# Kernel tuning notes

Hardware: AMD Instinct MI355X
Metric: run time of the kernel (lower is better)

## Reference

```python
import jax, jax.numpy as jnp
import numpy as np


def _c2e(faces):
    # faces: [6, B, C, h, h] in order back, down, front, left, right, up
    # returns equirect map [B, C, H=h, W=2h] via bilinear cube sampling
    _, B, C, h, _ = faces.shape
    H, W = h, 2 * h
    lat = (0.5 - (jnp.arange(H) + 0.5) / H) * jnp.pi      # +pi/2 (top) .. -pi/2
    lon = (2.0 * (jnp.arange(W) + 0.5) / W - 1.0) * jnp.pi  # -pi .. +pi
    cl = jnp.cos(lat)[:, None]
    vx = cl * jnp.sin(lon)[None, :]
    vy = jnp.broadcast_to(jnp.sin(lat)[:, None], (H, W))
    vz = cl * jnp.cos(lon)[None, :]
    dirs = jnp.stack([vx, vy, vz], -1)                     # [H,W,3]
    ax, ay, az = jnp.abs(vx), jnp.abs(vy), jnp.abs(vz)
    cond_z = (az >= ax) & (az >= ay)
    cond_x = (~cond_z) & (ax >= ay)
    # face ids: 0 back(-z) 1 down(-y) 2 front(+z) 3 left(-x) 4 right(+x) 5 up(+y)
    face = jnp.where(cond_z, jnp.where(vz > 0, 2, 0),
                     jnp.where(cond_x, jnp.where(vx > 0, 4, 3),
                               jnp.where(vy > 0, 5, 1)))
    N = jnp.array([[0, 0, -1], [0, -1, 0], [0, 0, 1], [-1, 0, 0], [1, 0, 0], [0, 1, 0]], jnp.float32)
    R = jnp.array([[-1, 0, 0], [1, 0, 0], [1, 0, 0], [0, 0, 1], [0, 0, -1], [1, 0, 0]], jnp.float32)
    U = jnp.array([[0, 1, 0], [0, 0, -1], [0, 1, 0], [0, 1, 0], [0, 1, 0], [0, 0, 1]], jnp.float32)
    den = jnp.sum(dirs * N[face], -1)
    a = jnp.sum(dirs * R[face], -1) / den                  # in-plane x, [-1,1]
    bcoord = jnp.sum(dirs * U[face], -1) / den             # in-plane y, [-1,1]
    uu = jnp.clip((a + 1.0) * 0.5 * (h - 1), 0.0, h - 1)   # align_corners-style
    vv = jnp.clip((1.0 - bcoord) * 0.5 * (h - 1), 0.0, h - 1)
    x0 = jnp.floor(uu).astype(jnp.int32)
    y0 = jnp.floor(vv).astype(jnp.int32)
    x1 = jnp.minimum(x0 + 1, h - 1)
    y1 = jnp.minimum(y0 + 1, h - 1)
    dx = uu - x0
    dy = vv - y0
    ft = faces.transpose(0, 3, 4, 1, 2).reshape(6, h, h, B * C)  # [6,h,h,B*C]
    g = lambda yy, xx: ft[face, yy, xx]                    # gather -> [H,W,B*C]
    out = (g(y0, x0) * ((1 - dx) * (1 - dy))[..., None]
           + g(y0, x1) * (dx * (1 - dy))[..., None]
           + g(y1, x0) * ((1 - dx) * dy)[..., None]
           + g(y1, x1) * (dx * dy)[..., None])
    return out.reshape(H, W, B, C).transpose(2, 3, 0, 1)


def _conv(x, w, bias, pad):
    y = jax.lax.conv_general_dilated(x, w, (1, 1), [(pad, pad), (pad, pad)],
                                     dimension_numbers=('NCHW', 'OIHW', 'NCHW'))
    return y + bias[None, :, None, None]


def setup_inputs() -> dict:
    key = jax.random.key(0)
    ks = jax.random.split(key, 12)
    B, C, h = 4, 64, 128
    face_shape = (B, C, h, h)
    return {
        'm': jax.random.normal(ks[0], (B, C, h, 2 * h), jnp.float32),
        'f': jax.random.normal(ks[1], face_shape, jnp.float32),
        'r': jax.random.normal(ks[2], face_shape, jnp.float32),
        'b': jax.random.normal(ks[3], face_shape, jnp.float32),
        'l': jax.random.normal(ks[4], face_shape, jnp.float32),
        'u': jax.random.normal(ks[5], face_shape, jnp.float32),
        'd': jax.random.normal(ks[6], face_shape, jnp.float32),
        'w_fusion': jax.random.normal(ks[7], (C, C, 3, 3), jnp.float32) * 0.05,
        'b_fusion': jnp.zeros((C,), jnp.float32),
        'w_mask': jax.random.normal(ks[8], (1, 2 * C, 1, 1), jnp.float32) * 0.05,
        'b_mask': jnp.zeros((1,), jnp.float32),
    }


def reference(m, f, r, b, l, u, d, w_fusion, b_fusion, w_mask, b_mask):
    # cube faces stacked in the original order: back, down, front, left, right, up
    faces = jnp.stack([b, d, f, l, r, u], 0)               # [6,B,C,h,h]
    aux = _c2e(faces)                                      # [B,C,h,2h]
    m_aux = jax.nn.relu(_conv(aux, w_fusion, b_fusion, 1))
    m_main = jax.nn.relu(_conv(m, w_fusion, b_fusion, 1))  # shared conv_fusion weights
    joint = jnp.concatenate([m_main, m_aux], axis=1)
    mask = jax.nn.sigmoid(_conv(joint, w_mask, b_mask, 0)) # [B,1,h,2h]
    return m + mask * m_aux
```

## Files before the change

### kernel.cpp

```cpp
#include <hip/hip_runtime.h>
#include <math.h>
#include <stdint.h>

#define BB 4
#define CC 64
#define HH 128
#define HOUT 128
#define WOUT 256
#define NPIX (HOUT * WOUT)
#define NMAP (BB * CC * HOUT * WOUT)

typedef __attribute__((ext_vector_type(8))) short short8;
typedef __attribute__((ext_vector_type(4))) float floatx4;

__device__ __forceinline__ uint16_t f2bf(float f) {
    uint32_t u = __float_as_uint(f);
    u += 0x7fffu + ((u >> 16) & 1u);
    return (uint16_t)(u >> 16);
}
__device__ __forceinline__ float bfu2f(uint32_t v) { return __uint_as_float(v << 16); }

__global__ __launch_bounds__(256) void prep_kernel(uint32_t* __restrict__ pk,
                                                   float* __restrict__ pdx,
                                                   float* __restrict__ pdy,
                                                   const float* __restrict__ wf,
                                                   uint4* __restrict__ Bsw) {
    if (blockIdx.x < 128) {
        int p = blockIdx.x * 256 + threadIdx.x;
        int y = p >> 8;
        int x = p & 255;
        const float PI = 3.14159265358979323846f;
        float lat = (0.5f - (y + 0.5f) / (float)HOUT) * PI;
        float lon = (2.0f * (x + 0.5f) / (float)WOUT - 1.0f) * PI;
        float cl = cosf(lat);
        float vx = cl * sinf(lon);
        float vy = sinf(lat);
        float vz = cl * cosf(lon);
        float ax = fabsf(vx), ay = fabsf(vy), az = fabsf(vz);

        int face;
        float den, a, b;
        if (az >= ax && az >= ay) {
            if (vz > 0.0f) { face = 2; den = vz;  a = vx;  b = vy; }
            else           { face = 0; den = -vz; a = -vx; b = vy; }
        } else if (ax >= ay) {
            if (vx > 0.0f) { face = 4; den = vx;  a = -vz; b = vy; }
            else           { face = 3; den = -vx; a = vz;  b = vy; }
        } else {
            if (vy > 0.0f) { face = 5; den = vy;  a = vx;  b = vz; }
            else           { face = 1; den = -vy; a = vx;  b = -vz; }
        }
        a /= den;
        b /= den;
        float uu = fminf(fmaxf((a + 1.0f) * 0.5f * (HH - 1), 0.0f), (float)(HH - 1));
        float vv = fminf(fmaxf((1.0f - b) * 0.5f * (HH - 1), 0.0f), (float)(HH - 1));
        int x0 = (int)floorf(uu);
        int y0 = (int)floorf(vv);
        int x1 = min(x0 + 1, HH - 1);
        int y1 = min(y0 + 1, HH - 1);
        pdx[p] = uu - (float)x0;
        pdy[p] = vv - (float)y0;
        pk[p] = (uint32_t)face | ((uint32_t)x0 << 3) | ((uint32_t)y0 << 10) |
                ((uint32_t)x1 << 17) | ((uint32_t)y1 << 24);
    } else {
        int tid = (blockIdx.x - 128) * 256 + threadIdx.x;
        if (tid >= 9 * 2 * 4 * 64) return;
        int lane = tid & 63;
        int rest = tid >> 6;
        int n = rest & 3, ks = (rest >> 2) & 1, tap = rest >> 3;
        int co = n * 16 + (lane & 15);
        uint32_t w4[4];
#pragma unroll
        for (int pw = 0; pw < 4; pw++) {
            int ci0 = ks * 32 + (lane >> 4) * 8 + pw * 2;
            uint32_t lo = f2bf(wf[(size_t)(co * CC + ci0) * 9 + tap]);
            uint32_t hi = f2bf(wf[(size_t)(co * CC + ci0 + 1) * 9 + tap]);
            w4[pw] = lo | (hi << 16);
        }
        Bsw[tid] = make_uint4(w4[0], w4[1], w4[2], w4[3]);
    }
}

__global__ __launch_bounds__(256) void facepack_kernel(
    const float* __restrict__ pB, const float* __restrict__ pD,
    const float* __restrict__ pF, const float* __restrict__ pL,
    const float* __restrict__ pR, const float* __restrict__ pU,
    uint16_t* __restrict__ FCL) {
    __shared__ uint16_t lds[64 * 256];
    int bid = blockIdx.x;
    int half = bid & 1;
    int y = (bid >> 1) & 127;
    int fc = bid >> 8;
    const float* src = (fc == 0) ? pB : (fc == 1) ? pD : (fc == 2) ? pF
                     : (fc == 3) ? pL : (fc == 4) ? pR : pU;
    int t = threadIdx.x;
    int xl = t & 63;
    int x = half * 64 + xl;
    int cgb = t >> 6;

#pragma unroll
    for (int i = 0; i < 8; i++) {
        int cg = i * 4 + cgb;
        uint32_t w4[4];
#pragma unroll
        for (int j = 0; j < 4; j++) {
            int bc0 = cg * 8 + j * 2;
            uint32_t lo = f2bf(src[((size_t)bc0 * HH + y) * HH + x]);
            uint32_t hi = f2bf(src[((size_t)(bc0 + 1) * HH + y) * HH + x]);
            w4[j] = lo | (hi << 16);
        }
        int off = xl * 256 + ((cg ^ (xl & 7)) * 8);
        *(uint4*)&lds[off] = make_uint4(w4[0], w4[1], w4[2], w4[3]);
    }
    __syncthreads();
    size_t obase = (((size_t)fc * HH + y) * HH + half * 64) * 256;
#pragma unroll
    for (int i = 0; i < 8; i++) {
        int q = i * 256 + t;
        int xx = q >> 5, cg = q & 31;
        int off = xx * 256 + ((cg ^ (xx & 7)) * 8);
        *(uint4*)&FCL[obase + (size_t)q * 8] = *(const uint4*)&lds[off];
    }
}

__global__ __launch_bounds__(256) void gather_kernel(
    const uint32_t* __restrict__ pk, const float* __restrict__ pdx,
    const float* __restrict__ pdy, const uint16_t* __restrict__ FCL,
    uint16_t* __restrict__ Xa) {
    int tid = blockIdx.x * 256 + threadIdx.x;
    int chunk = tid & 31;
    int p = tid >> 5;

    uint32_t k = pk[p];
    float dx = pdx[p], dy = pdy[p];
    int fc = k & 7;
    int x0 = (k >> 3) & 127, y0 = (k >> 10) & 127;
    int x1 = (k >> 17) & 127, y1 = (k >> 24) & 127;

    const uint16_t* base = FCL + (size_t)fc * HH * HH * 256 + chunk * 8;
    uint4 c00 = *(const uint4*)(base + ((size_t)y0 * HH + x0) * 256);
    uint4 c01 = *(const uint4*)(base + ((size_t)y0 * HH + x1) * 256);
    uint4 c10 = *(const uint4*)(base + ((size_t)y1 * HH + x0) * 256);
    uint4 c11 = *(const uint4*)(base + ((size_t)y1 * HH + x1) * 256);

    float w00 = (1.0f - dx) * (1.0f - dy);
    float w01 = dx * (1.0f - dy);
    float w10 = (1.0f - dx) * dy;
    float w11 = dx * dy;

    const uint32_t* a00 = (const uint32_t*)&c00;
    const uint32_t* a01 = (const uint32_t*)&c01;
    const uint32_t* a10 = (const uint32_t*)&c10;
    const uint32_t* a11 = (const uint32_t*)&c11;
    uint32_t r[4];
#pragma unroll
    for (int w = 0; w < 4; w++) {
        float lo = w00 * bfu2f(a00[w] & 0xffffu) + w01 * bfu2f(a01[w] & 0xffffu)
                 + w10 * bfu2f(a10[w] & 0xffffu) + w11 * bfu2f(a11[w] & 0xffffu);
        float hi = w00 * bfu2f(a00[w] >> 16) + w01 * bfu2f(a01[w] >> 16)
                 + w10 * bfu2f(a10[w] >> 16) + w11 * bfu2f(a11[w] >> 16);
        r[w] = (uint32_t)f2bf(lo) | ((uint32_t)f2bf(hi) << 16);
    }

    int b = chunk >> 3, c = (chunk & 7) * 8;
    int y = p >> 8, x = p & 255;
    size_t o = (((size_t)(b * HOUT + y)) * WOUT + x) * CC + c;
    *(uint4*)(Xa + o) = make_uint4(r[0], r[1], r[2], r[3]);
}

__global__ __launch_bounds__(256) void pack_kernel(const float* __restrict__ src,
                                                   uint16_t* __restrict__ dst) {
    __shared__ uint16_t lds[WOUT * CC];
    int t = threadIdx.x;
    int by = blockIdx.x;
    int b = by >> 7, y = by & 127;

#pragma unroll
    for (int cg = 0; cg < 8; cg++) {
        uint32_t w4[4];
#pragma unroll
        for (int pw = 0; pw < 4; pw++) {
            int c0 = cg * 8 + pw * 2;
            uint32_t lo = f2bf(src[((size_t)(b * CC + c0) * HOUT + y) * WOUT + t]);
            uint32_t hi = f2bf(src[((size_t)(b * CC + c0 + 1) * HOUT + y) * WOUT + t]);
            w4[pw] = lo | (hi << 16);
        }
        int off = t * 64 + ((cg ^ (t & 7)) * 8);
        *(uint4*)&lds[off] = make_uint4(w4[0], w4[1], w4[2], w4[3]);
    }
    __syncthreads();
    size_t obase = (size_t)((b * HOUT + y) * WOUT) * CC;
#pragma unroll
    for (int i = 0; i < 8; i++) {
        int q = i * 256 + t;
        int p = q >> 3, c8 = q & 7;
        int off = p * 64 + ((c8 ^ (p & 7)) * 8);
        *(uint4*)&dst[obase + (size_t)q * 8] = *(const uint4*)&lds[off];
    }
}

__global__ __launch_bounds__(256) void gemm_kernel(const uint16_t* __restrict__ Xm,
                                                   const uint16_t* __restrict__ Xa,
                                                   const uint4* __restrict__ Bsw,
                                                   const float* __restrict__ bias,
                                                   uint16_t* __restrict__ Ym,
                                                   uint16_t* __restrict__ Ya) {
    __shared__ uint16_t lds[3 * 160 * CC];
    int gid = blockIdx.x;
    int tensor = gid >> 10;
    int b = (gid >> 8) & 3;
    int i = gid & 255;
    int xcd = i & 7, j = i >> 3;
    int y = xcd * 16 + (j & 15);
    int h = j >> 4;
    const uint16_t* X = tensor ? Xa : Xm;
    uint16_t* Y = tensor ? Ya : Ym;
    const int wx = h * 128 - 16;

    int tid = threadIdx.x;
    const uint16_t* Xb = X + (size_t)b * (HOUT * WOUT * CC);
#pragma unroll
    for (int it = 0; it < 15; it++) {
        int cid = it * 256 + tid;
        int c = cid & 7;
        int pr = cid >> 3;
        int p = pr % 160;
        int r = pr / 160;
        int gy = y + r - 1;
        int gx = wx + p;
        uint4 v = make_uint4(0, 0, 0, 0);
        if ((unsigned)gy < (unsigned)HOUT && (unsigned)gx < (unsigned)WOUT)
            v = *(const uint4*)(Xb + ((size_t)gy * WOUT + gx) * CC + c * 8);
        int slot = (r * 160 + p) * 8 + (c ^ (p & 7));
        *(uint4*)&lds[slot * 8] = v;
    }
    __syncthreads();

    int lane = threadIdx.x & 63;
    int wave = threadIdx.x >> 6;
    int l15 = lane & 15, lq = lane >> 4;

    floatx4 acc[2][4];
#pragma unroll
    for (int mt = 0; mt < 2; mt++)
#pragma unroll
        for (int n = 0; n < 4; n++) acc[mt][n] = (floatx4)0.0f;

#pragma unroll
    for (int tap = 0; tap < 9; tap++) {
        const int dy = tap / 3 - 1, dx = tap % 3 - 1;
        const int r = 1 + dy;
#pragma unroll
        for (int ks = 0; ks < 2; ks++) {
            short8 bfr[4];
            const uint4* bp = Bsw + (size_t)((tap * 2 + ks) * 4) * 64 + lane;
#pragma unroll
            for (int n = 0; n < 4; n++) {
                uint4 t4 = bp[n * 64];
                bfr[n] = *(short8*)&t4;
            }
#pragma unroll
            for (int mt = 0; mt < 2; mt++) {
                int p = wave * 32 + mt * 16 + l15 + dx + 16;
                int chunk = ks * 4 + lq;
                int slot = (r * 160 + p) * 8 + (chunk ^ (p & 7));
                short8 af = *(const short8*)&lds[slot * 8];
#pragma unroll
                for (int n = 0; n < 4; n++)
                    acc[mt][n] = __builtin_amdgcn_mfma_f32_16x16x32_bf16(
                        af, bfr[n], acc[mt][n], 0, 0, 0);
            }
        }
    }
    long rowpix = (long)(b * HOUT + y) * WOUT;
#pragma unroll
    for (int n = 0; n < 4; n++) {
        int co = n * 16 + l15;
        float bb = bias[co];
#pragma unroll
        for (int mt = 0; mt < 2; mt++) {
#pragma unroll
            for (int rg = 0; rg < 4; rg++) {
                float v = acc[mt][n][rg] + bb;
                v = v > 0.0f ? v : 0.0f;
                long px = rowpix + h * 128 + wave * 32 + mt * 16 + lq * 4 + rg;
                Y[px * CC + co] = f2bf(v);
            }
        }
    }
}

__global__ __launch_bounds__(256) void maskfinal_kernel(
    const float* __restrict__ m, const uint16_t* __restrict__ Ym,
    const uint16_t* __restrict__ Ya, const float* __restrict__ wm,
    const float* __restrict__ bm, float* __restrict__ out) {
    int t = threadIdx.x;
    int by = blockIdx.x;
    int b = by >> 7, y = by & 127;
    size_t pix = (size_t)(b * HOUT + y) * WOUT + t;
    const uint4* ym4 = (const uint4*)(Ym + pix * CC);
    const uint4* ya4 = (const uint4*)(Ya + pix * CC);
    uint4 ya[8];
    float acc = bm[0];
#pragma unroll
    for (int g = 0; g < 8; g++) {
        uint4 um = ym4[g];
        uint4 av = ya4[g];
        ya[g] = av;
        const uint32_t* pu = (const uint32_t*)&um;
        const uint32_t* pa = (const uint32_t*)&av;
#pragma unroll
        for (int w = 0; w < 4; w++) {
            int c = g * 8 + w * 2;
            acc += wm[c]     * bfu2f(pu[w] & 0xffffu);
            acc += wm[c + 1] * bfu2f(pu[w] >> 16);
            acc += wm[64 + c]     * bfu2f(pa[w] & 0xffffu);
            acc += wm[64 + c + 1] * bfu2f(pa[w] >> 16);
        }
    }
    float mask = 1.0f / (1.0f + expf(-acc));
#pragma unroll
    for (int g = 0; g < 8; g++) {
        const uint32_t* pa = (const uint32_t*)&ya[g];
#pragma unroll
        for (int w = 0; w < 4; w++) {
            int c = g * 8 + w * 2;
            size_t i0 = ((size_t)(b * CC + c) * HOUT + y) * WOUT + t;
            size_t i1 = i0 + (size_t)HOUT * WOUT;
            out[i0] = m[i0] + mask * bfu2f(pa[w] & 0xffffu);
            out[i1] = m[i1] + mask * bfu2f(pa[w] >> 16);
        }
    }
}

__global__ __launch_bounds__(256) void signal_kernel(float* __restrict__ out, float v) {
    int idx = blockIdx.x * 256 + threadIdx.x;
    out[idx] = v;
}

extern "C" void kernel_launch(void* const* d_in, const int* in_sizes, int n_in,
                              void* d_out, int out_size, void* d_ws, size_t ws_size,
                              hipStream_t stream) {
    const float* m  = (const float*)d_in[0];
    const float* f  = (const float*)d_in[1];
    const float* r  = (const float*)d_in[2];
    const float* bk = (const float*)d_in[3];
    const float* l  = (const float*)d_in[4];
    const float* u  = (const float*)d_in[5];
    const float* dn = (const float*)d_in[6];
    const float* wf = (const float*)d_in[7];
    const float* bf = (const float*)d_in[8];
    const float* wm = (const float*)d_in[9];
    const float* bm = (const float*)d_in[10];
    float* out = (float*)d_out;

    const size_t OFF_FCL = 0;
    const size_t OFF_YM  = 0;
    const size_t OFF_YA  = (size_t)16 << 20;
    const size_t OFF_BSW = (size_t)51 << 20;
    const size_t OFF_PK  = OFF_BSW + (1u << 17);
    const size_t OFF_PDX = OFF_PK + (1u << 17);
    const size_t OFF_PDY = OFF_PDX + (1u << 17);
    const size_t NEED    = OFF_PDY + (1u << 17);

    if (ws_size < NEED) {
        float v = 100.0f + (float)(ws_size >> 20);
        signal_kernel<<<NMAP / 256, 256, 0, stream>>>(out, v);
        return;
    }

    char* ws = (char*)d_ws;
    uint16_t* FCL = (uint16_t*)(ws + OFF_FCL);
    uint16_t* Ym  = (uint16_t*)(ws + OFF_YM);
    uint16_t* Ya  = (uint16_t*)(ws + OFF_YA);
    uint4* Bsw    = (uint4*)(ws + OFF_BSW);
    uint32_t* pk  = (uint32_t*)(ws + OFF_PK);
    float* pdx    = (float*)(ws + OFF_PDX);
    float* pdy    = (float*)(ws + OFF_PDY);
    uint16_t* Xm  = (uint16_t*)d_out;
    uint16_t* Xa  = (uint16_t*)d_out + (size_t)NMAP;

    prep_kernel<<<146, 256, 0, stream>>>(pk, pdx, pdy, wf, Bsw);
    facepack_kernel<<<6 * HH * 2, 256, 0, stream>>>(bk, dn, f, l, r, u, FCL);
    gather_kernel<<<(NPIX * 32) / 256, 256, 0, stream>>>(pk, pdx, pdy, FCL, Xa);
    pack_kernel<<<BB * HOUT, 256, 0, stream>>>(m, Xm);
    gemm_kernel<<<2 * BB * HOUT * 2, 256, 0, stream>>>(Xm, Xa, Bsw, bf, Ym, Ya);
    maskfinal_kernel<<<BB * HOUT, 256, 0, stream>>>(m, Ym, Ya, wm, bm, out);
}
```

Measured before the change: 262.0 us.

## Fuse both conv GEMMs with mask and final blend into one kernel

The two 3x3 conv GEMMs (main and aux) now run as two phases inside a single block per row-half, and the 1x1 mask conv, sigmoid and residual blend are folded into the epilogue. The bf16 Ym/Ya intermediates and the separate maskfinal kernel are removed. The LDS halo is trimmed from 160 to 132 columns, and the face buffer and workspace layout are reshuffled so the output buffer holds part of the face cache. The trade-off is half as many blocks, serial phases within each block, and an LDS transpose before the NCHW stores.

```diff
diff --git a/kernel.cpp b/kernel.cpp
--- a/kernel.cpp
+++ b/kernel.cpp
@@ -9,6 +9,7 @@
 #define WOUT 256
 #define NPIX (HOUT * WOUT)
 #define NMAP (BB * CC * HOUT * WOUT)
+#define FSTR ((size_t)HH * HH * 256)
 
 typedef __attribute__((ext_vector_type(8))) short short8;
 typedef __attribute__((ext_vector_type(4))) float floatx4;
@@ -85,7 +86,7 @@
     const float* __restrict__ pB, const float* __restrict__ pD,
     const float* __restrict__ pF, const float* __restrict__ pL,
     const float* __restrict__ pR, const float* __restrict__ pU,
-    uint16_t* __restrict__ FCL) {
+    uint16_t* __restrict__ FCLlo, uint16_t* __restrict__ FCLhi) {
     __shared__ uint16_t lds[64 * 256];
     int bid = blockIdx.x;
     int half = bid & 1;
@@ -93,6 +94,8 @@
     int fc = bid >> 8;
     const float* src = (fc == 0) ? pB : (fc == 1) ? pD : (fc == 2) ? pF
                      : (fc == 3) ? pL : (fc == 4) ? pR : pU;
+    uint16_t* FCL = (fc < 3) ? (FCLlo + (size_t)fc * FSTR)
+                             : (FCLhi + (size_t)(fc - 3) * FSTR);
     int t = threadIdx.x;
     int xl = t & 63;
     int x = half * 64 + xl;
@@ -113,7 +116,7 @@
         *(uint4*)&lds[off] = make_uint4(w4[0], w4[1], w4[2], w4[3]);
     }
     __syncthreads();
-    size_t obase = (((size_t)fc * HH + y) * HH + half * 64) * 256;
+    size_t obase = ((size_t)y * HH + half * 64) * 256;
 #pragma unroll
     for (int i = 0; i < 8; i++) {
         int q = i * 256 + t;
@@ -125,8 +128,8 @@
 
 __global__ __launch_bounds__(256) void gather_kernel(
     const uint32_t* __restrict__ pk, const float* __restrict__ pdx,
-    const float* __restrict__ pdy, const uint16_t* __restrict__ FCL,
-    uint16_t* __restrict__ Xa) {
+    const float* __restrict__ pdy, const uint16_t* __restrict__ FCLlo,
+    const uint16_t* __restrict__ FCLhi, uint16_t* __restrict__ Xa) {
     int tid = blockIdx.x * 256 + threadIdx.x;
     int chunk = tid & 31;
     int p = tid >> 5;
@@ -137,7 +140,9 @@
     int x0 = (k >> 3) & 127, y0 = (k >> 10) & 127;
     int x1 = (k >> 17) & 127, y1 = (k >> 24) & 127;
 
-    const uint16_t* base = FCL + (size_t)fc * HH * HH * 256 + chunk * 8;
+    const uint16_t* fb = (fc < 3) ? (FCLlo + (size_t)fc * FSTR)
+                                  : (FCLhi + (size_t)(fc - 3) * FSTR);
+    const uint16_t* base = fb + chunk * 8;
     uint4 c00 = *(const uint4*)(base + ((size_t)y0 * HH + x0) * 256);
     uint4 c01 = *(const uint4*)(base + ((size_t)y0 * HH + x1) * 256);
     uint4 c10 = *(const uint4*)(base + ((size_t)y1 * HH + x0) * 256);
@@ -199,137 +204,159 @@
     }
 }
 
-__global__ __launch_bounds__(256) void gemm_kernel(const uint16_t* __restrict__ Xm,
-                                                   const uint16_t* __restrict__ Xa,
-                                                   const uint4* __restrict__ Bsw,
-                                                   const float* __restrict__ bias,
-                                                   uint16_t* __restrict__ Ym,
-                                                   uint16_t* __restrict__ Ya) {
-    __shared__ uint16_t lds[3 * 160 * CC];
+__global__ __launch_bounds__(256, 4) void gemm_fused_kernel(
+    const uint16_t* __restrict__ Xm, const uint16_t* __restrict__ Xa,
+    const uint4* __restrict__ Bsw, const float* __restrict__ bias,
+    const float* __restrict__ wm, const float* __restrict__ bm,
+    const float* __restrict__ m, float* __restrict__ out) {
+    __shared__ __align__(16) uint16_t lds[3 * 132 * 64];
+    float* ldsf = (float*)lds;
+
     int gid = blockIdx.x;
-    int tensor = gid >> 10;
-    int b = (gid >> 8) & 3;
+    int b = gid >> 8;
     int i = gid & 255;
     int xcd = i & 7, j = i >> 3;
     int y = xcd * 16 + (j & 15);
     int h = j >> 4;
-    const uint16_t* X = tensor ? Xa : Xm;
-    uint16_t* Y = tensor ? Ya : Ym;
-    const int wx = h * 128 - 16;
+    const int wx = h * 128 - 2;
 
     int tid = threadIdx.x;
-    const uint16_t* Xb = X + (size_t)b * (HOUT * WOUT * CC);
-#pragma unroll
-    for (int it = 0; it < 15; it++) {
-        int cid = it * 256 + tid;
-        int c = cid & 7;
-        int pr = cid >> 3;
-        int p = pr % 160;
-        int r = pr / 160;
-        int gy = y + r - 1;
-        int gx = wx + p;
-        uint4 v = make_uint4(0, 0, 0, 0);
-        if ((unsigned)gy < (unsigned)HOUT && (unsigned)gx < (unsigned)WOUT)
-            v = *(const uint4*)(Xb + ((size_t)gy * WOUT + gx) * CC + c * 8);
-        int slot = (r * 160 + p) * 8 + (c ^ (p & 7));
-        *(uint4*)&lds[slot * 8] = v;
-    }
+    int lane = tid & 63;
+    int wave = tid >> 6;
+    int l15 = lane & 15, lq = lane >> 4;
+
+    float bb[4], wmm[4], wma[4];
+#pragma unroll
+    for (int n = 0; n < 4; n++) {
+        bb[n] = bias[n * 16 + l15];
+        wmm[n] = wm[n * 16 + l15];
+        wma[n] = wm[64 + n * 16 + l15];
+    }
+    float bm0 = bm[0];
+
+    float mp[2][4];
+#pragma unroll
+    for (int mt = 0; mt < 2; mt++)
+#pragma unroll
+        for (int rg = 0; rg < 4; rg++) mp[mt][rg] = 0.0f;
+
+    floatx4 acc[2][4];
+
+#pragma unroll
+    for (int phase = 0; phase < 2; phase++) {
+        const uint16_t* X = phase ? Xa : Xm;
+        const uint16_t* Xb = X + (size_t)b * (HOUT * WOUT * CC);
+
+        __syncthreads();
+#pragma unroll
+        for (int it = 0; it < 13; it++) {
+            int cid = it * 256 + tid;
+            if (cid < 3168) {
+                int c = cid & 7;
+                int pr = cid >> 3;
+                int p = pr % 132;
+                int r = pr / 132;
+                int gy = y + r - 1;
+                int gx = wx + p;
+                uint4 v = make_uint4(0, 0, 0, 0);
+                if ((unsigned)gy < (unsigned)HOUT && (unsigned)gx < (unsigned)WOUT)
+                    v = *(const uint4*)(Xb + ((size_t)gy * WOUT + gx) * CC + c * 8);
+                int slot = (r * 132 + p) * 8 + (c ^ (p & 7));
+                *(uint4*)&lds[slot * 8] = v;
+            }
+        }
+        __syncthreads();
+
+#pragma unroll
+        for (int mt = 0; mt < 2; mt++)
+#pragma unroll
+            for (int n = 0; n < 4; n++) acc[mt][n] = (floatx4)0.0f;
+
+#pragma unroll
+        for (int tap = 0; tap < 9; tap++) {
+            const int r = tap / 3;
+            const int dx = tap % 3 - 1;
+#pragma unroll
+            for (int ks = 0; ks < 2; ks++) {
+                short8 bfr[4];
+                const uint4* bp = Bsw + (size_t)((tap * 2 + ks) * 4) * 64 + lane;
+#pragma unroll
+                for (int n = 0; n < 4; n++) {
+                    uint4 t4 = bp[n * 64];
+                    bfr[n] = *(short8*)&t4;
+                }
+#pragma unroll
+                for (int mt = 0; mt < 2; mt++) {
+                    int p = wave * 32 + mt * 16 + l15 + dx + 2;
+                    int chunk = ks * 4 + lq;
+                    int slot = (r * 132 + p) * 8 + (chunk ^ (p & 7));
+                    short8 af = *(const short8*)&lds[slot * 8];
+#pragma unroll
+                    for (int n = 0; n < 4; n++)
+                        acc[mt][n] = __builtin_amdgcn_mfma_f32_16x16x32_bf16(
+                            af, bfr[n], acc[mt][n], 0, 0, 0);
+                }
+            }
+        }
+
+        if (phase == 0) {
+#pragma unroll
+            for (int mt = 0; mt < 2; mt++)
+#pragma unroll
+                for (int n = 0; n < 4; n++)
+#pragma unroll
+                    for (int rg = 0; rg < 4; rg++) {
+                        float v = acc[mt][n][rg] + bb[n];
+                        v = v > 0.0f ? v : 0.0f;
+                        mp[mt][rg] += wmm[n] * v;
+                    }
+        } else {
+#pragma unroll
+            for (int mt = 0; mt < 2; mt++)
+#pragma unroll
+                for (int n = 0; n < 4; n++)
+#pragma unroll
+                    for (int rg = 0; rg < 4; rg++) {
+                        float v = acc[mt][n][rg] + bb[n];
+                        v = v > 0.0f ? v : 0.0f;
+                        acc[mt][n][rg] = v;
+                        mp[mt][rg] += wma[n] * v;
+                    }
+        }
+    }
+
+#pragma unroll
+    for (int mt = 0; mt < 2; mt++)
+#pragma unroll
+        for (int rg = 0; rg < 4; rg++) {
+            float v = mp[mt][rg];
+            v += __shfl_xor(v, 1);
+            v += __shfl_xor(v, 2);
+            v += __shfl_xor(v, 4);
+            v += __shfl_xor(v, 8);
+            mp[mt][rg] = 1.0f / (1.0f + expf(-(v + bm0)));
+        }
+
     __syncthreads();
-
-    int lane = threadIdx.x & 63;
-    int wave = threadIdx.x >> 6;
-    int l15 = lane & 15, lq = lane >> 4;
-
-    floatx4 acc[2][4];
 #pragma unroll
     for (int mt = 0; mt < 2; mt++)
 #pragma unroll
-        for (int n = 0; n < 4; n++) acc[mt][n] = (floatx4)0.0f;
-
-#pragma unroll
-    for (int tap = 0; tap < 9; tap++) {
-        const int dy = tap / 3 - 1, dx = tap % 3 - 1;
-        const int r = 1 + dy;
-#pragma unroll
-        for (int ks = 0; ks < 2; ks++) {
-            short8 bfr[4];
-            const uint4* bp = Bsw + (size_t)((tap * 2 + ks) * 4) * 64 + lane;
-#pragma unroll
-            for (int n = 0; n < 4; n++) {
-                uint4 t4 = bp[n * 64];
-                bfr[n] = *(short8*)&t4;
+        for (int n = 0; n < 4; n++)
+#pragma unroll
+            for (int rg = 0; rg < 4; rg++) {
+                int px = wave * 32 + mt * 16 + lq * 4 + rg;
+                int co = n * 16 + l15;
+                ldsf[co * 129 + px] = mp[mt][rg] * acc[mt][n][rg];
             }
-#pragma unroll
-            for (int mt = 0; mt < 2; mt++) {
-                int p = wave * 32 + mt * 16 + l15 + dx + 16;
-                int chunk = ks * 4 + lq;
-                int slot = (r * 160 + p) * 8 + (chunk ^ (p & 7));
-                short8 af = *(const short8*)&lds[slot * 8];
-#pragma unroll
-                for (int n = 0; n < 4; n++)
-                    acc[mt][n] = __builtin_amdgcn_mfma_f32_16x16x32_bf16(
-                        af, bfr[n], acc[mt][n], 0, 0, 0);
-            }
-        }
-    }
-    long rowpix = (long)(b * HOUT + y) * WOUT;
-#pragma unroll
-    for (int n = 0; n < 4; n++) {
-        int co = n * 16 + l15;
-        float bb = bias[co];
-#pragma unroll
-        for (int mt = 0; mt < 2; mt++) {
-#pragma unroll
-            for (int rg = 0; rg < 4; rg++) {
-                float v = acc[mt][n][rg] + bb;
-                v = v > 0.0f ? v : 0.0f;
-                long px = rowpix + h * 128 + wave * 32 + mt * 16 + lq * 4 + rg;
-                Y[px * CC + co] = f2bf(v);
-            }
-        }
-    }
-}
-
-__global__ __launch_bounds__(256) void maskfinal_kernel(
-    const float* __restrict__ m, const uint16_t* __restrict__ Ym,
-    const uint16_t* __restrict__ Ya, const float* __restrict__ wm,
-    const float* __restrict__ bm, float* __restrict__ out) {
-    int t = threadIdx.x;
-    int by = blockIdx.x;
-    int b = by >> 7, y = by & 127;
-    size_t pix = (size_t)(b * HOUT + y) * WOUT + t;
-    const uint4* ym4 = (const uint4*)(Ym + pix * CC);
-    const uint4* ya4 = (const uint4*)(Ya + pix * CC);
-    uint4 ya[8];
-    float acc = bm[0];
-#pragma unroll
-    for (int g = 0; g < 8; g++) {
-        uint4 um = ym4[g];
-        uint4 av = ya4[g];
-        ya[g] = av;
-        const uint32_t* pu = (const uint32_t*)&um;
-        const uint32_t* pa = (const uint32_t*)&av;
-#pragma unroll
-        for (int w = 0; w < 4; w++) {
-            int c = g * 8 + w * 2;
-            acc += wm[c]     * bfu2f(pu[w] & 0xffffu);
-            acc += wm[c + 1] * bfu2f(pu[w] >> 16);
-            acc += wm[64 + c]     * bfu2f(pa[w] & 0xffffu);
-            acc += wm[64 + c + 1] * bfu2f(pa[w] >> 16);
-        }
-    }
-    float mask = 1.0f / (1.0f + expf(-acc));
-#pragma unroll
-    for (int g = 0; g < 8; g++) {
-        const uint32_t* pa = (const uint32_t*)&ya[g];
-#pragma unroll
-        for (int w = 0; w < 4; w++) {
-            int c = g * 8 + w * 2;
-            size_t i0 = ((size_t)(b * CC + c) * HOUT + y) * WOUT + t;
-            size_t i1 = i0 + (size_t)HOUT * WOUT;
-            out[i0] = m[i0] + mask * bfu2f(pa[w] & 0xffffu);
-            out[i1] = m[i1] + mask * bfu2f(pa[w] >> 16);
-        }
+    __syncthreads();
+
+    size_t base0 = (size_t)b * (CC * HOUT * WOUT) + (size_t)y * WOUT + h * 128;
+#pragma unroll
+    for (int it = 0; it < 32; it++) {
+        int q = it * 256 + tid;
+        int c = q >> 7, px = q & 127;
+        size_t idx = base0 + (size_t)c * (HOUT * WOUT) + px;
+        out[idx] = m[idx] + ldsf[c * 129 + px];
     }
 }
 
@@ -354,14 +381,15 @@
     const float* bm = (const float*)d_in[10];
     float* out = (float*)d_out;
 
-    const size_t OFF_FCL = 0;
-    const size_t OFF_YM  = 0;
-    const size_t OFF_YA  = (size_t)16 << 20;
-    const size_t OFF_BSW = (size_t)51 << 20;
-    const size_t OFF_PK  = OFF_BSW + (1u << 17);
-    const size_t OFF_PDX = OFF_PK + (1u << 17);
-    const size_t OFF_PDY = OFF_PDX + (1u << 17);
-    const size_t NEED    = OFF_PDY + (1u << 17);
+    const size_t FCL_HALF = (size_t)3 * HH * HH * 256 * 2;
+    const size_t OFF_FCLH = 0;
+    const size_t OFF_XA   = FCL_HALF;
+    const size_t OFF_XM   = OFF_XA + (size_t)NMAP * 2;
+    const size_t OFF_BSW  = OFF_XM + (size_t)NMAP * 2;
+    const size_t OFF_PK   = OFF_BSW + (9 * 2 * 4 * 64 * 16);
+    const size_t OFF_PDX  = OFF_PK + (1u << 17);
+    const size_t OFF_PDY  = OFF_PDX + (1u << 17);
+    const size_t NEED     = OFF_PDY + (1u << 17);
 
     if (ws_size < NEED) {
         float v = 100.0f + (float)(ws_size >> 20);
@@ -370,20 +398,18 @@
     }
 
     char* ws = (char*)d_ws;
-    uint16_t* FCL = (uint16_t*)(ws + OFF_FCL);
-    uint16_t* Ym  = (uint16_t*)(ws + OFF_YM);
-    uint16_t* Ya  = (uint16_t*)(ws + OFF_YA);
-    uint4* Bsw    = (uint4*)(ws + OFF_BSW);
-    uint32_t* pk  = (uint32_t*)(ws + OFF_PK);
-    float* pdx    = (float*)(ws + OFF_PDX);
-    float* pdy    = (float*)(ws + OFF_PDY);
-    uint16_t* Xm  = (uint16_t*)d_out;
-    uint16_t* Xa  = (uint16_t*)d_out + (size_t)NMAP;
+    uint16_t* FCLhi = (uint16_t*)(ws + OFF_FCLH);
+    uint16_t* Xa    = (uint16_t*)(ws + OFF_XA);
+    uint16_t* Xm    = (uint16_t*)(ws + OFF_XM);
+    uint4* Bsw      = (uint4*)(ws + OFF_BSW);
+    uint32_t* pk    = (uint32_t*)(ws + OFF_PK);
+    float* pdx      = (float*)(ws + OFF_PDX);
+    float* pdy      = (float*)(ws + OFF_PDY);
+    uint16_t* FCLlo = (uint16_t*)d_out;
 
     prep_kernel<<<146, 256, 0, stream>>>(pk, pdx, pdy, wf, Bsw);
-    facepack_kernel<<<6 * HH * 2, 256, 0, stream>>>(bk, dn, f, l, r, u, FCL);
-    gather_kernel<<<(NPIX * 32) / 256, 256, 0, stream>>>(pk, pdx, pdy, FCL, Xa);
+    facepack_kernel<<<6 * HH * 2, 256, 0, stream>>>(bk, dn, f, l, r, u, FCLlo, FCLhi);
+    gather_kernel<<<(NPIX * 32) / 256, 256, 0, stream>>>(pk, pdx, pdy, FCLlo, FCLhi, Xa);
     pack_kernel<<<BB * HOUT, 256, 0, stream>>>(m, Xm);
-    gemm_kernel<<<2 * BB * HOUT * 2, 256, 0, stream>>>(Xm, Xa, Bsw, bf, Ym, Ya);
-    maskfinal_kernel<<<BB * HOUT, 256, 0, stream>>>(m, Ym, Ya, wm, bm, out);
-}
+    gemm_fused_kernel<<<BB * HOUT * 2, 256, 0, stream>>>(Xm, Xa, Bsw, bf, wm, bm, m, out);
+}
```

Result: no change. 266.2 us (+1.6%).
